# Kernel tuning notes

Measured on AMD Instinct MI355X. Metric: run time of the kernel, lower is better.

The kernel has to match this reference:

```python
import jax, jax.numpy as jnp
import numpy as np

NUM_HEADS = 8
H_DIM = 24
COORDS_DIM = 3
NUM_W_PER_DIST = 8
BLOCK_SIZE = 128
N_HASHES = 3
N = 32768
HASH_DIM = H_DIM + (COORDS_DIM - 1) + 2  # q/k augmented with RPE coordinate terms


def layernorm(x, g, b, eps=1e-5):
    mu = x.mean(-1, keepdims=True)
    var = ((x - mu) ** 2).mean(-1, keepdims=True)
    return (x - mu) * jax.lax.rsqrt(var + eps) * g + b


def setup_inputs() -> dict:
    key = jax.random.key(0)
    ks = jax.random.split(key, 16)
    d, H = H_DIM, NUM_HEADS
    s = lambda i, shape, scale: jax.random.normal(ks[i], shape, jnp.float32) * scale
    return {
        "x": s(0, (N, d), 1.0),
        "coords": jax.random.uniform(ks[1], (N, COORDS_DIM), jnp.float32),
        "norm1_g": jnp.ones((d,), jnp.float32),
        "norm1_b": jnp.zeros((d,), jnp.float32),
        "Wq": s(2, (d, H * d), d ** -0.5),
        "Wk": s(3, (d, H * d), d ** -0.5),
        "Wv": s(4, (d, H * d), d ** -0.5),
        "w_rpe_W": s(5, (H * d, (COORDS_DIM - 1) * NUM_W_PER_DIST), 0.3),
        "Wo": s(6, (H * d, d), (H * d) ** -0.5),
        "bo": jnp.zeros((d,), jnp.float32),
        "norm2_g": jnp.ones((d,), jnp.float32),
        "norm2_b": jnp.zeros((d,), jnp.float32),
        "ff_W1": s(7, (d, d), d ** -0.5),
        "ff_b1": jnp.zeros((d,), jnp.float32),
        "ff_W2": s(8, (d, d), d ** -0.5),
        "ff_b2": jnp.zeros((d,), jnp.float32),
        "alphas": s(9, (N_HASHES, H, HASH_DIM), 1.0),  # E2LSH projection vectors
    }


def hept_attention(q, k, v, coords, w_rpe_W, alphas):
    # q,k,v: [n, H*d]. HEPT: fold RPE exp(-w*||dp||^2) into augmented q/k, then
    # n_hashes rounds of LSH sort + block-local attention, combined by softmax
    # over each round's log-normalizer (Reformer-style).
    n = q.shape[0]
    H, d, B = NUM_HEADS, H_DIM, BLOCK_SIZE
    nb = n // B
    q = q.reshape(n, H, d).transpose(1, 0, 2) * (d ** -0.5)  # [H,n,d]
    k = k.reshape(n, H, d).transpose(1, 0, 2)
    v = v.reshape(n, H, d).transpose(1, 0, 2)
    # per-head non-negative distance weights from w_rpe (mixture collapsed)
    Wm = w_rpe_W.reshape(H, d, COORDS_DIM - 1, NUM_W_PER_DIST)
    w = jnp.mean(Wm, axis=(1, 3)) ** 2                        # [H, c-1]
    p = coords[:, 1:]                                          # [n, c-1]
    sqn = jnp.einsum("hc,nc,nc->hn", w, p, p)                # w*||p||^2
    qp = jnp.sqrt(2.0) * jnp.sqrt(w)[:, None, :] * p[None]     # [H,n,c-1]
    ones = jnp.ones((H, n, 1), q.dtype)
    # q_hat.k_hat = q.k + 2*w*p_i.p_j - w|p_i|^2 - w|p_j|^2 = q.k - w*||p_i-p_j||^2
    q_hat = jnp.concatenate([q, qp, -sqn[..., None], ones], -1)  # [H,n,HASH_DIM]
    k_hat = jnp.concatenate([k, qp, ones, -sqn[..., None]], -1)
    outs, zs = [], []
    for r in range(N_HASHES):
        a = alphas[r]                                          # [H, HASH_DIM]
        iq = jnp.argsort(jnp.einsum("hne,he->hn", q_hat, a), -1)
        ik = jnp.argsort(jnp.einsum("hne,he->hn", k_hat, a), -1)
        qs = jnp.take_along_axis(q_hat, iq[..., None], 1).reshape(H, nb, B, -1)
        ks = jnp.take_along_axis(k_hat, ik[..., None], 1).reshape(H, nb, B, -1)
        vs = jnp.take_along_axis(v, ik[..., None], 1).reshape(H, nb, B, d)
        logits = jnp.einsum("hbqe,hbke->hbqk", qs, ks)         # [H,nb,B,B]
        z = jax.nn.logsumexp(logits, -1).reshape(H, n)
        o = jnp.einsum("hbqk,hbkd->hbqd", jax.nn.softmax(logits, -1), vs).reshape(H, n, d)
        inv = jnp.argsort(iq, -1)                              # unsort to input order
        outs.append(jnp.take_along_axis(o, inv[..., None], 1))
        zs.append(jnp.take_along_axis(z, inv, 1))
    wts = jax.nn.softmax(jnp.stack(zs), axis=0)[..., None]     # [R,H,n,1]
    out = (jnp.stack(outs) * wts).sum(0)                       # [H,n,d]
    return out.transpose(1, 0, 2).reshape(n, H * d)


def reference(x, coords, norm1_g, norm1_b, Wq, Wk, Wv, w_rpe_W, Wo, bo,
              norm2_g, norm2_b, ff_W1, ff_b1, ff_W2, ff_b2, alphas):
    xn = layernorm(x, norm1_g, norm1_b)
    q, k, v = xn @ Wq, xn @ Wk, xn @ Wv
    aggr = hept_attention(q, k, v, coords, w_rpe_W, alphas) @ Wo + bo
    x = x + aggr  # dropout is identity in eval mode
    h = layernorm(x, norm2_g, norm2_b)
    ff = jax.nn.relu(h @ ff_W1 + ff_b1) @ ff_W2 + ff_b2
    return x + ff
```

## Files before the change

kernel.cpp:

```cpp
#include <hip/hip_runtime.h>
#include <math.h>

#define NPT 32768
#define NH 8
#define HD 24
#define EDIM 28
#define NHASH 3
#define NSEG 48
#define NRH 24

typedef unsigned long long u64;
typedef unsigned short ushort;
typedef __attribute__((__vector_size__(8 * sizeof(short)))) short bf16x8;
typedef __attribute__((__vector_size__(4 * sizeof(float)))) float floatx4;

__device__ __forceinline__ ushort f2bf(float f) {
    unsigned u = __float_as_uint(f);
    unsigned r = u + 0x7FFF + ((u >> 16) & 1);
    return (ushort)(r >> 16);
}
__device__ __forceinline__ float us2f(ushort u) {
    return __uint_as_float(((unsigned)u) << 16);
}

__global__ __launch_bounds__(256) void k0b(
    const float* __restrict__ wrpe, const float* __restrict__ Wq,
    const float* __restrict__ Wk, const float* __restrict__ alphas,
    double* __restrict__ w64, double* __restrict__ cqp64,
    double* __restrict__ Aq, double* __restrict__ Ak, double* __restrict__ ct) {
    __shared__ double sw[16], sc[16];
    int t = threadIdx.x;
    if (t < 16) {
        int h = t >> 1, c = t & 1;
        double s = 0.0;
        for (int i = 0; i < 24; i++)
            for (int j = 0; j < 8; j++)
                s += (double)wrpe[(h * 24 + i) * 16 + c * 8 + j];
        double m = s / 192.0;
        sw[t] = m * m;
        sc[t] = sqrt(2.0) * fabs(m);
        w64[t] = sw[t];
        cqp64[t] = sc[t];
    }
    __syncthreads();
    const double QSCALE = 1.0 / sqrt(24.0);
    for (int idx = t; idx < 24 * NRH; idx += 256) {
        int i = idx / NRH, rh = idx % NRH;
        int h = rh & 7;
        double aq = 0.0, ak = 0.0;
        for (int e = 0; e < 24; e++) {
            double al = (double)alphas[rh * 28 + e];
            aq += (double)Wq[i * 192 + h * 24 + e] * al;
            ak += (double)Wk[i * 192 + h * 24 + e] * al;
        }
        Aq[idx] = aq * QSCALE;
        Ak[idx] = ak;
    }
    if (t < NRH) {
        int h = t & 7;
        ct[t * 4 + 0] = (double)alphas[t * 28 + 24] * sc[h * 2 + 0];
        ct[t * 4 + 1] = (double)alphas[t * 28 + 25] * sc[h * 2 + 1];
        ct[t * 4 + 2] = (double)alphas[t * 28 + 26];
        ct[t * 4 + 3] = (double)alphas[t * 28 + 27];
    }
}

__global__ __launch_bounds__(256) void k1b(
    const float* __restrict__ x, const float* __restrict__ g,
    const float* __restrict__ b, float* __restrict__ xnf) {
    __shared__ float sGB[48];
    int t = threadIdx.x;
    if (t < 24) { sGB[t] = g[t]; sGB[24 + t] = b[t]; }
    __syncthreads();
    int wv = t >> 6, l = t & 63;
    int half = l >> 5, e = l & 31;
    for (int it = 0; it < 8; it++) {
        int n = blockIdx.x * 64 + it * 8 + wv * 2 + half;
        float xv = (e < 24) ? x[(u64)n * 24 + e] : 0.f;
        float s = xv;
        s += __shfl_xor(s, 1); s += __shfl_xor(s, 2); s += __shfl_xor(s, 4);
        s += __shfl_xor(s, 8); s += __shfl_xor(s, 16);
        float mu = s * (1.0f / 24.0f);
        float d = (e < 24) ? (xv - mu) : 0.f;
        float v = d * d;
        v += __shfl_xor(v, 1); v += __shfl_xor(v, 2); v += __shfl_xor(v, 4);
        v += __shfl_xor(v, 8); v += __shfl_xor(v, 16);
        float rstd = 1.0f / sqrtf(v * (1.0f / 24.0f) + 1e-5f);
        if (e < 24) xnf[(u64)n * 24 + e] = d * rstd * sGB[e] + sGB[24 + e];
    }
}

__global__ __launch_bounds__(512) void k2s(
    const float* __restrict__ x, const float* __restrict__ n1g,
    const float* __restrict__ n1b, const float* __restrict__ coords,
    const double* __restrict__ Aq, const double* __restrict__ Ak,
    const double* __restrict__ ct, const double* __restrict__ w64,
    u64* __restrict__ keys) {
    __shared__ double sA[2][24][NRH];
    __shared__ double sCt[NRH][4];
    __shared__ double sW64[16];
    __shared__ double sGB[48];
    __shared__ double sXn[8][24];
    int t = threadIdx.x;
    for (int i = t; i < 24 * NRH; i += 512) sA[0][i / NRH][i % NRH] = Aq[i];
    for (int i = t; i < 24 * NRH; i += 512) sA[1][i / NRH][i % NRH] = Ak[i];
    for (int i = t; i < NRH * 4; i += 512) sCt[i / 4][i % 4] = ct[i];
    if (t < 16) sW64[t] = w64[t];
    if (t < 24) { sGB[t] = (double)n1g[t]; sGB[24 + t] = (double)n1b[t]; }
    __syncthreads();
    int wv = t >> 6, l = t & 63;
    for (int g = 0; g < 8; g++) {
        int n = blockIdx.x * 64 + g * 8 + wv;
        double xv = (l < 24) ? (double)x[(u64)n * 24 + l] : 0.0;
        double s = xv;
        s += __shfl_xor(s, 1); s += __shfl_xor(s, 2); s += __shfl_xor(s, 4);
        s += __shfl_xor(s, 8); s += __shfl_xor(s, 16);
        double mu = s / 24.0;
        double d = (l < 24) ? (xv - mu) : 0.0;
        double v2 = d * d;
        v2 += __shfl_xor(v2, 1); v2 += __shfl_xor(v2, 2); v2 += __shfl_xor(v2, 4);
        v2 += __shfl_xor(v2, 8); v2 += __shfl_xor(v2, 16);
        double rstd = 1.0 / sqrt(v2 / 24.0 + 1e-5);
        if (l < 24) sXn[wv][l] = d * rstd * sGB[l] + sGB[24 + l];
        double p0 = (double)coords[(u64)n * 3 + 1];
        double p1 = (double)coords[(u64)n * 3 + 2];
        if (l < 2 * NRH) {
            int qk = l / NRH, rh = l % NRH;
            int h = rh & 7;
            double sqn = sW64[2 * h] * p0 * p0 + sW64[2 * h + 1] * p1 * p1;
            double acc = sCt[rh][0] * p0 + sCt[rh][1] * p1;
            acc += qk ? (sCt[rh][2] - sqn * sCt[rh][3]) : (sCt[rh][3] - sqn * sCt[rh][2]);
            for (int i = 0; i < 24; i++) acc += sXn[wv][i] * sA[qk][i][rh];
            u64 u = (u64)__double_as_longlong(acc);
            if (u >> 63) u = ~u; else u |= 0x8000000000000000ULL;
            u64 key = (u & ~(u64)32767) | (u64)n;
            keys[(u64)l * NPT + n] = key;
        }
    }
}

#define K2P_PTS 64
__global__ __launch_bounds__(640) void k2p(
    const float* __restrict__ xnf,
    const float* __restrict__ Wq, const float* __restrict__ Wk,
    const float* __restrict__ Wv, const float* __restrict__ coords,
    const double* __restrict__ w64, const double* __restrict__ cqp64,
    ushort* __restrict__ qhatB, ushort* __restrict__ khatB, ushort* __restrict__ varrB) {
    int t = threadIdx.x;
    int n0 = blockIdx.x * K2P_PTS;
    if (t < 576) {
        int m = t / 192, jj = t % 192;
        const float* W = (m == 0) ? Wq : ((m == 1) ? Wk : Wv);
        float wc[24];
#pragma unroll
        for (int i = 0; i < 24; i++) wc[i] = W[i * 192 + jj];
        const float scale = (m == 0) ? (float)(1.0 / sqrt(24.0)) : 1.0f;
        int h = jj / 24, e = jj % 24;
        ushort* outp = (m == 0) ? qhatB : ((m == 1) ? khatB : varrB);
        ushort* obase = outp + (u64)h * NPT * 32 + e;
        for (int p = 0; p < K2P_PTS; p++) {
            int n = n0 + p;
            const float* xr = xnf + (u64)n * 24;
            float acc = 0.f;
#pragma unroll
            for (int i = 0; i < 24; i++) acc += xr[i] * wc[i];
            obase[(u64)n * 32] = f2bf(acc * scale);
        }
    } else {
        int l = t - 576;
        int h2 = l >> 3, e2 = 24 + (l & 7);
        double c0 = cqp64[h2 * 2], c1 = cqp64[h2 * 2 + 1];
        double wa = w64[h2 * 2], wb = w64[h2 * 2 + 1];
        ushort* qb = qhatB + (u64)h2 * NPT * 32 + e2;
        ushort* kb = khatB + (u64)h2 * NPT * 32 + e2;
        for (int p = 0; p < K2P_PTS; p++) {
            int n = n0 + p;
            double p0 = (double)coords[(u64)n * 3 + 1];
            double p1 = (double)coords[(u64)n * 3 + 2];
            float qv, kv;
            if (e2 < 26) {
                int c = e2 - 24;
                float qp = (float)((c ? c1 : c0) * (c ? p1 : p0));
                qv = qp; kv = qp;
            } else if (e2 < 28) {
                double sqn = wa * p0 * p0 + wb * p1 * p1;
                if (e2 == 26) { qv = (float)(-sqn); kv = 1.0f; }
                else          { qv = 1.0f; kv = (float)(-sqn); }
            } else {
                qv = 0.0f; kv = 0.0f;
            }
            qb[(u64)n * 32] = f2bf(qv);
            kb[(u64)n * 32] = f2bf(kv);
        }
    }
}

__device__ __forceinline__ u64 shflx64(u64 v, int d) {
    int lo = __shfl_xor((int)(unsigned)v, d);
    int hi = __shfl_xor((int)(unsigned)(v >> 32), d);
    return ((u64)(unsigned)hi << 32) | (unsigned)lo;
}
__device__ __forceinline__ void cswap(u64& a, u64& b, bool up) {
    if ((a > b) == up) { u64 tmp = a; a = b; b = tmp; }
}
__device__ __forceinline__ u64* sslot(u64* s, int i) {
    int a = i << 3;
    a ^= ((a >> 9) & 7) << 4;
    return (u64*)((char*)s + a);
}
__device__ __forceinline__ void reg_passes(u64 e[8], int ib, int K, int jmax) {
    for (int j = jmax; j >= 1; j >>= 1) {
#pragma unroll
        for (int k = 0; k < 8; k++)
            if ((k & j) == 0) cswap(e[k], e[k | j], ((ib + k) & K) == 0);
    }
}
__device__ __forceinline__ void shfl_passes(u64 e[8], int t, int segoff, int K, int jhi, int jlo) {
    for (int j = jhi; j >= jlo; j >>= 1) {
        int d = j >> 3;
        bool lower = (t & d) == 0;
        bool up = ((segoff + ((t & ~d) << 3)) & K) == 0;
        bool keepmin = (lower == up);
#pragma unroll
        for (int k = 0; k < 8; k++) {
            u64 o = shflx64(e[k], d);
            bool ownsm = e[k] < o;
            e[k] = (ownsm == keepmin) ? e[k] : o;
        }
    }
}

__global__ __launch_bounds__(1024) void sort_local_full(u64* keys) {
    __shared__ u64 s[8192];
    int t = threadIdx.x;
    u64 gbase = (u64)blockIdx.x * 8192;
    int segoff = (int)(gbase & 32767);
    int ib = segoff + t * 8;
    u64 e[8];
#pragma unroll
    for (int k = 0; k < 8; k++) e[k] = keys[gbase + t * 8 + k];
    reg_passes(e, ib, 2, 1);
    reg_passes(e, ib, 4, 2);
    reg_passes(e, ib, 8, 4);
    for (int K = 16; K <= 512; K <<= 1) {
        shfl_passes(e, t, segoff, K, K >> 1, 8);
        reg_passes(e, ib, K, 4);
    }
#pragma unroll
    for (int k = 0; k < 8; k++) *sslot(s, t * 8 + k) = e[k];
    __syncthreads();
    for (int K = 1024; K <= 8192; K <<= 1) {
        for (int j = K >> 1; j >= 512; j >>= 1) {
            for (int p = t; p < 4096; p += 1024) {
                int i = ((p & ~(j - 1)) << 1) | (p & (j - 1));
                int i2 = i | j;
                bool up = (((segoff + i) & K) == 0);
                u64 a = *sslot(s, i), b = *sslot(s, i2);
                if ((a > b) == up) { *sslot(s, i) = b; *sslot(s, i2) = a; }
            }
            __syncthreads();
        }
#pragma unroll
        for (int k = 0; k < 8; k++) e[k] = *sslot(s, t * 8 + k);
        shfl_passes(e, t, segoff, K, 256, 8);
        reg_passes(e, ib, K, 4);
        if (K < 8192) {
#pragma unroll
            for (int k = 0; k < 8; k++) *sslot(s, t * 8 + k) = e[k];
            __syncthreads();
        } else {
#pragma unroll
            for (int k = 0; k < 8; k++) keys[gbase + t * 8 + k] = e[k];
        }
    }
}

__global__ __launch_bounds__(1024) void sort_local_tail(u64* keys, int K, int minj) {
    __shared__ u64 s[8192];
    int t = threadIdx.x;
    u64 gbase = (u64)blockIdx.x * 8192;
    int segoff = (int)(gbase & 32767);
    int ib = segoff + t * 8;
    for (int i = t; i < 8192; i += 1024) *sslot(s, i) = keys[gbase + i];
    __syncthreads();
    for (int j = 4096; j >= 512; j >>= 1) {
        for (int p = t; p < 4096; p += 1024) {
            int i = ((p & ~(j - 1)) << 1) | (p & (j - 1));
            int i2 = i | j;
            bool up = (((segoff + i) & K) == 0);
            u64 a = *sslot(s, i), b = *sslot(s, i2);
            if ((a > b) == up) { *sslot(s, i) = b; *sslot(s, i2) = a; }
        }
        __syncthreads();
    }
    u64 e[8];
#pragma unroll
    for (int k = 0; k < 8; k++) e[k] = *sslot(s, t * 8 + k);
    shfl_passes(e, t, segoff, K, 256, minj >= 8 ? minj : 8);
    if (minj < 8) reg_passes(e, ib, K, 4);
#pragma unroll
    for (int k = 0; k < 8; k++) keys[gbase + t * 8 + k] = e[k];
}

__global__ void sort_global_pass(u64* keys, int k, int j) {
    int p = blockIdx.x * blockDim.x + threadIdx.x;
    if (p >= NSEG * NPT / 2) return;
    int i = ((p & ~(j - 1)) << 1) | (p & (j - 1));
    int l2 = i | j;
    bool up = (((i & 32767) & k) == 0);
    u64 a = keys[i], b = keys[l2];
    if ((a > b) == up) { keys[i] = b; keys[l2] = a; }
}

__global__ void sort_global2(u64* keys) {
    int p = blockIdx.x * blockDim.x + threadIdx.x;
    if (p >= NSEG * 8192) return;
    int seg = p >> 13, c = p & 8191;
    u64 base = (u64)seg * 32768 + c;
    u64 e0 = keys[base];
    u64 e1 = keys[base + 8192];
    u64 e2 = keys[base + 16384];
    u64 e3 = keys[base + 24576];
    u64 tmp;
    if (e0 > e2) { tmp = e0; e0 = e2; e2 = tmp; }
    if (e1 > e3) { tmp = e1; e1 = e3; e3 = tmp; }
    if (e0 > e1) { tmp = e0; e0 = e1; e1 = tmp; }
    if (e2 > e3) { tmp = e2; e2 = e3; e3 = tmp; }
    keys[base] = e0;
    keys[base + 8192] = e1;
    keys[base + 16384] = e2;
    keys[base + 24576] = e3;
}

#define VT_STRIDE 136
#define P_STRIDE 72
__global__ __launch_bounds__(256, 4) void k3_attn(
    const u64* __restrict__ keys, const ushort* __restrict__ qhatB,
    const ushort* __restrict__ khatB, const ushort* __restrict__ varrB,
    ushort* __restrict__ ozB) {
    int rh3 = blockIdx.x % 24;
    int b = blockIdx.x / 24;
    int h = rh3 & 7, r = rh3 >> 3;
    __shared__ __align__(16) char smem[6528 + 18432 + 1024];
    short* sVt = (short*)smem;
    short* sP  = (short*)(smem + 6528);
    int* qidx  = (int*)(smem + 6528 + 18432);
    int* kidx  = qidx + 128;
    int t = threadIdx.x;
    int segQ = r * 8 + h, segK = 24 + r * 8 + h;
    if (t < 128) {
        qidx[t] = (int)(keys[(u64)segQ * NPT + b * 128 + t] & 32767ULL);
    } else {
        int i = t - 128;
        kidx[i] = (int)(keys[(u64)segK * NPT + b * 128 + i] & 32767ULL);
    }
    __syncthreads();

    int wave = t >> 6, L = t & 63;
    int quad = L >> 4, n16 = L & 15;

    const bf16x8* Qg = (const bf16x8*)(qhatB + (u64)h * NPT * 32);
    const bf16x8* Kg = (const bf16x8*)(khatB + (u64)h * NPT * 32);
    bf16x8 afr[2];
#pragma unroll
    for (int rtg = 0; rtg < 2; rtg++) {
        int qi = qidx[wave * 32 + rtg * 16 + n16];
        afr[rtg] = Qg[(u64)qi * 4 + quad];
    }
    bf16x8 bfr[8];
#pragma unroll
    for (int ct = 0; ct < 8; ct++) {
        int ki = kidx[ct * 16 + n16];
        bfr[ct] = Kg[(u64)ki * 4 + quad];
    }
    if (t < 128) {
        int ki = kidx[t];
        const bf16x8* vr = (const bf16x8*)(varrB + ((u64)h * NPT + ki) * 32);
        bf16x8 v0 = vr[0], v1 = vr[1], v2 = vr[2];
#pragma unroll
        for (int e = 0; e < 8; e++) {
            sVt[e * VT_STRIDE + t]        = v0[e];
            sVt[(8 + e) * VT_STRIDE + t]  = v1[e];
            sVt[(16 + e) * VT_STRIDE + t] = v2[e];
        }
    }
    __syncthreads();

    floatx4 acc[2][8];
#pragma unroll
    for (int rtg = 0; rtg < 2; rtg++)
#pragma unroll
        for (int ct = 0; ct < 8; ct++)
            acc[rtg][ct] = (floatx4){0.f, 0.f, 0.f, 0.f};
#pragma unroll
    for (int ct = 0; ct < 8; ct++) {
#pragma unroll
        for (int rtg = 0; rtg < 2; rtg++)
            acc[rtg][ct] = __builtin_amdgcn_mfma_f32_16x16x32_bf16(afr[rtg], bfr[ct], acc[rtg][ct], 0, 0, 0);
    }

    float mrow[2][4], srow[2][4];
#pragma unroll
    for (int rtg = 0; rtg < 2; rtg++) {
#pragma unroll
        for (int rg = 0; rg < 4; rg++) {
            float m = -1e30f;
#pragma unroll
            for (int ct = 0; ct < 8; ct++) m = fmaxf(m, acc[rtg][ct][rg]);
            m = fmaxf(m, __shfl_xor(m, 1));
            m = fmaxf(m, __shfl_xor(m, 2));
            m = fmaxf(m, __shfl_xor(m, 4));
            m = fmaxf(m, __shfl_xor(m, 8));
            mrow[rtg][rg] = m;
            float s = 0.0f;
            int row = wave * 32 + rtg * 16 + quad * 4 + rg;
#pragma unroll
            for (int ct = 0; ct < 8; ct++) {
                float p = __expf(acc[rtg][ct][rg] - m);
                s += p;
                if (ct < 4) sP[row * P_STRIDE + ct * 16 + n16] = (short)f2bf(p);
            }
            s += __shfl_xor(s, 1);
            s += __shfl_xor(s, 2);
            s += __shfl_xor(s, 4);
            s += __shfl_xor(s, 8);
            srow[rtg][rg] = s;
        }
    }

    floatx4 occ[2][2];
#pragma unroll
    for (int rtg = 0; rtg < 2; rtg++)
#pragma unroll
        for (int ct2 = 0; ct2 < 2; ct2++)
            occ[rtg][ct2] = (floatx4){0.f, 0.f, 0.f, 0.f};
#pragma unroll
    for (int ks = 0; ks < 2; ks++) {
        bf16x8 bv[2], av[2];
#pragma unroll
        for (int ct2 = 0; ct2 < 2; ct2++)
            bv[ct2] = *(const bf16x8*)(sVt + (ct2 * 16 + n16) * VT_STRIDE + ks * 32 + quad * 8);
#pragma unroll
        for (int rtg = 0; rtg < 2; rtg++)
            av[rtg] = *(const bf16x8*)(sP + (wave * 32 + rtg * 16 + n16) * P_STRIDE + ks * 32 + quad * 8);
#pragma unroll
        for (int rtg = 0; rtg < 2; rtg++)
#pragma unroll
            for (int ct2 = 0; ct2 < 2; ct2++)
                occ[rtg][ct2] = __builtin_amdgcn_mfma_f32_16x16x32_bf16(av[rtg], bv[ct2], occ[rtg][ct2], 0, 0, 0);
    }
#pragma unroll
    for (int rtg = 0; rtg < 2; rtg++) {
#pragma unroll
        for (int rg = 0; rg < 4; rg++) {
            int row = wave * 32 + rtg * 16 + quad * 4 + rg;
#pragma unroll
            for (int ct = 4; ct < 8; ct++) {
                float p = __expf(acc[rtg][ct][rg] - mrow[rtg][rg]);
                sP[row * P_STRIDE + (ct - 4) * 16 + n16] = (short)f2bf(p);
            }
        }
    }
#pragma unroll
    for (int ks = 2; ks < 4; ks++) {
        bf16x8 bv[2], av[2];
#pragma unroll
        for (int ct2 = 0; ct2 < 2; ct2++)
            bv[ct2] = *(const bf16x8*)(sVt + (ct2 * 16 + n16) * VT_STRIDE + ks * 32 + quad * 8);
#pragma unroll
        for (int rtg = 0; rtg < 2; rtg++)
            av[rtg] = *(const bf16x8*)(sP + (wave * 32 + rtg * 16 + n16) * P_STRIDE + (ks - 2) * 32 + quad * 8);
#pragma unroll
        for (int rtg = 0; rtg < 2; rtg++)
#pragma unroll
            for (int ct2 = 0; ct2 < 2; ct2++)
                occ[rtg][ct2] = __builtin_amdgcn_mfma_f32_16x16x32_bf16(av[rtg], bv[ct2], occ[rtg][ct2], 0, 0, 0);
    }

#pragma unroll
    for (int rtg = 0; rtg < 2; rtg++) {
#pragma unroll
        for (int rg = 0; rg < 4; rg++) {
            int row = wave * 32 + rtg * 16 + quad * 4 + rg;
            int oi = qidx[row];
            float inv = 1.0f / srow[rtg][rg];
            ushort* orow = ozB + ((u64)segQ * NPT + oi) * 32;
#pragma unroll
            for (int ct2 = 0; ct2 < 2; ct2++) {
                int col = ct2 * 16 + n16;
                if (col < 24) orow[col] = f2bf(occ[rtg][ct2][rg] * inv);
            }
            if (n16 == 0)
                *(float*)(orow + 24) = mrow[rtg][rg] + __logf(srow[rtg][rg]);
        }
    }
}

#define K4PTS 32
#define AT_STR 196
__global__ __launch_bounds__(256) void k4_final(
    const ushort* __restrict__ ozB,
    const float* __restrict__ x,
    const float* __restrict__ Wo, const float* __restrict__ bo,
    const float* __restrict__ g2, const float* __restrict__ b2,
    const float* __restrict__ W1, const float* __restrict__ b1f,
    const float* __restrict__ W2, const float* __restrict__ b2f,
    float* __restrict__ out) {
    __shared__ __align__(16) float sWoT[24][AT_STR];
    __shared__ float sW1[24 * 24], sW2[24 * 24];
    __shared__ float sB[5 * 24];
    __shared__ __align__(16) float attn[K4PTS][AT_STR];
    __shared__ float xrow[K4PTS][25];
    __shared__ float h2row[K4PTS][25];
    __shared__ float ffrow[K4PTS][25];
    int t = threadIdx.x;
    int base = blockIdx.x * K4PTS;
    for (int i = t; i < 4608; i += 256) sWoT[i % 24][i / 24] = Wo[i];
    for (int i = t; i < 576; i += 256) { sW1[i] = W1[i]; sW2[i] = W2[i]; }
    if (t < 24) {
        sB[t] = bo[t]; sB[24 + t] = g2[t]; sB[48 + t] = b2[t];
        sB[72 + t] = b1f[t]; sB[96 + t] = b2f[t];
    }
    {
        int p = t >> 3, h = t & 7;
        int n = base + p;
        const ushort* r0 = ozB + ((u64)(0 * 8 + h) * NPT + n) * 32;
        const ushort* r1 = ozB + ((u64)(1 * 8 + h) * NPT + n) * 32;
        const ushort* r2 = ozB + ((u64)(2 * 8 + h) * NPT + n) * 32;
        float z0 = *(const float*)(r0 + 24);
        float z1 = *(const float*)(r1 + 24);
        float z2 = *(const float*)(r2 + 24);
        float zm = fmaxf(z0, fmaxf(z1, z2));
        float e0 = __expf(z0 - zm), e1 = __expf(z1 - zm), e2 = __expf(z2 - zm);
        float inv = 1.0f / (e0 + e1 + e2);
        float w0 = e0 * inv, w1 = e1 * inv, w2 = e2 * inv;
#pragma unroll
        for (int e = 0; e < 24; e++)
            attn[p][h * 24 + e] = w0 * us2f(r0[e]) + w1 * us2f(r1[e]) + w2 * us2f(r2[e]);
    }
    __syncthreads();
    int p = t >> 3, oe = t & 7;
    int n = base + p;
    {
        const floatx4* ap = (const floatx4*)&attn[p][0];
        const floatx4* w0p = (const floatx4*)&sWoT[oe][0];
        const floatx4* w1p = (const floatx4*)&sWoT[oe + 8][0];
        const floatx4* w2p = (const floatx4*)&sWoT[oe + 16][0];
        floatx4 A0 = {0.f, 0.f, 0.f, 0.f}, A1 = A0, A2 = A0;
        for (int ii = 0; ii < 48; ii++) {
            floatx4 av = ap[ii];
            A0 += av * w0p[ii];
            A1 += av * w1p[ii];
            A2 += av * w2p[ii];
        }
        float a0 = A0[0] + A0[1] + A0[2] + A0[3];
        float a1 = A1[0] + A1[1] + A1[2] + A1[3];
        float a2 = A2[0] + A2[1] + A2[2] + A2[3];
        xrow[p][oe]      = x[n * 24 + oe]      + a0 + sB[oe];
        xrow[p][oe + 8]  = x[n * 24 + oe + 8]  + a1 + sB[oe + 8];
        xrow[p][oe + 16] = x[n * 24 + oe + 16] + a2 + sB[oe + 16];
    }
    float mu, rstd;
    {
        float s = xrow[p][oe] + xrow[p][oe + 8] + xrow[p][oe + 16];
        s += __shfl_xor(s, 1); s += __shfl_xor(s, 2); s += __shfl_xor(s, 4);
        mu = s / 24.0f;
        float v0 = xrow[p][oe] - mu, v1 = xrow[p][oe + 8] - mu, v2 = xrow[p][oe + 16] - mu;
        float v = v0 * v0 + v1 * v1 + v2 * v2;
        v += __shfl_xor(v, 1); v += __shfl_xor(v, 2); v += __shfl_xor(v, 4);
        rstd = 1.0f / sqrtf(v / 24.0f + 1e-5f);
    }
    h2row[p][oe]      = (xrow[p][oe] - mu)      * rstd * sB[24 + oe]      + sB[48 + oe];
    h2row[p][oe + 8]  = (xrow[p][oe + 8] - mu)  * rstd * sB[24 + oe + 8]  + sB[48 + oe + 8];
    h2row[p][oe + 16] = (xrow[p][oe + 16] - mu) * rstd * sB[24 + oe + 16] + sB[48 + oe + 16];
    {
        float a0 = sB[72 + oe], a1 = sB[72 + oe + 8], a2 = sB[72 + oe + 16];
        for (int i = 0; i < 24; i++) {
            float hi = h2row[p][i];
            a0 += hi * sW1[i * 24 + oe];
            a1 += hi * sW1[i * 24 + oe + 8];
            a2 += hi * sW1[i * 24 + oe + 16];
        }
        ffrow[p][oe]      = fmaxf(a0, 0.f);
        ffrow[p][oe + 8]  = fmaxf(a1, 0.f);
        ffrow[p][oe + 16] = fmaxf(a2, 0.f);
    }
    {
        float a0 = sB[96 + oe], a1 = sB[96 + oe + 8], a2 = sB[96 + oe + 16];
        for (int i = 0; i < 24; i++) {
            float fi = ffrow[p][i];
            a0 += fi * sW2[i * 24 + oe];
            a1 += fi * sW2[i * 24 + oe + 8];
            a2 += fi * sW2[i * 24 + oe + 16];
        }
        out[n * 24 + oe]      = xrow[p][oe]      + a0;
        out[n * 24 + oe + 8]  = xrow[p][oe + 8]  + a1;
        out[n * 24 + oe + 16] = xrow[p][oe + 16] + a2;
    }
}

extern "C" void kernel_launch(void* const* d_in, const int* in_sizes, int n_in,
                              void* d_out, int out_size, void* d_ws, size_t ws_size,
                              hipStream_t stream) {
    const float* x      = (const float*)d_in[0];
    const float* coords = (const float*)d_in[1];
    const float* n1g    = (const float*)d_in[2];
    const float* n1b    = (const float*)d_in[3];
    const float* Wq     = (const float*)d_in[4];
    const float* Wk     = (const float*)d_in[5];
    const float* Wv     = (const float*)d_in[6];
    const float* wrpe   = (const float*)d_in[7];
    const float* Wo     = (const float*)d_in[8];
    const float* bo     = (const float*)d_in[9];
    const float* n2g    = (const float*)d_in[10];
    const float* n2b    = (const float*)d_in[11];
    const float* W1     = (const float*)d_in[12];
    const float* b1     = (const float*)d_in[13];
    const float* W2     = (const float*)d_in[14];
    const float* b2     = (const float*)d_in[15];
    const float* alphas = (const float*)d_in[16];

    char* ws = (char*)d_ws;
    size_t off = 0;
    auto alloc = [&](size_t bytes) -> void* {
        void* p = ws + off;
        off = (off + bytes + 255) & ~(size_t)255;
        return p;
    };
    double* w64   = (double*)alloc(256);
    double* cqp   = (double*)alloc(256);
    double* Aq    = (double*)alloc(24 * NRH * 8);
    double* Ak    = (double*)alloc(24 * NRH * 8);
    double* ct    = (double*)alloc(NRH * 4 * 8);
    float*  xnf   = (float*)alloc((size_t)NPT * 24 * 4);
    ushort* qhatB = (ushort*)alloc((size_t)NH * NPT * 32 * 2);
    ushort* khatB = (ushort*)alloc((size_t)NH * NPT * 32 * 2);
    ushort* varrB = (ushort*)alloc((size_t)NH * NPT * 32 * 2);
    u64*    keys  = (u64*)alloc((size_t)NSEG * NPT * 8);
    ushort* ozB   = (ushort*)alloc((size_t)NHASH * NH * NPT * 32 * 2);
    if (off > ws_size) return;

    k0b<<<1, 256, 0, stream>>>(wrpe, Wq, Wk, alphas, w64, cqp, Aq, Ak, ct);
    k1b<<<NPT / 64, 256, 0, stream>>>(x, n1g, n1b, xnf);
    k2s<<<NPT / 64, 512, 0, stream>>>(x, n1g, n1b, coords, Aq, Ak, ct, w64, keys);
    k2p<<<NPT / K2P_PTS, 640, 0, stream>>>(xnf, Wq, Wk, Wv, coords, w64, cqp,
                                           qhatB, khatB, varrB);
    sort_local_full<<<192, 1024, 0, stream>>>(keys);
    sort_global_pass<<<3072, 256, 0, stream>>>(keys, 16384, 8192);
    sort_local_tail<<<192, 1024, 0, stream>>>(keys, 16384, 1);
    sort_global2<<<NSEG * 8192 / 256, 256, 0, stream>>>(keys);
    sort_local_tail<<<192, 1024, 0, stream>>>(keys, 32768, 128);
    k3_attn<<<256 * 8 * 3, 256, 0, stream>>>(keys, qhatB, khatB, varrB, ozB);
    k4_final<<<NPT / K4PTS, 256, 0, stream>>>(ozB, x, Wo, bo, n2g, n2b,
                                              W1, b1, W2, b2, (float*)d_out);
}
```

Measured before the change: 321.1 us.

## Fuse layernorm into key kernel, fold global sort pass into local tail, vectorize FFN

Removes the separate layernorm kernel k1b by having k2s also write the float normalized activations. The bitonic global compare-exchange pass with j=8192 is folded into the following local tail kernel: each block loads its own chunk and the partner chunk and keeps the min or max. The FFN matmuls in k4_final use transposed, padded weight tiles and floatx4 dot products. The result is two fewer launches and less global traffic, at the cost of redundant partner reads in the fused sort and a different float summation order in the FFN.

```diff
diff --git a/kernel.cpp b/kernel.cpp
--- a/kernel.cpp
+++ b/kernel.cpp
@@ -65,37 +65,12 @@
     }
 }
 
-__global__ __launch_bounds__(256) void k1b(
-    const float* __restrict__ x, const float* __restrict__ g,
-    const float* __restrict__ b, float* __restrict__ xnf) {
-    __shared__ float sGB[48];
-    int t = threadIdx.x;
-    if (t < 24) { sGB[t] = g[t]; sGB[24 + t] = b[t]; }
-    __syncthreads();
-    int wv = t >> 6, l = t & 63;
-    int half = l >> 5, e = l & 31;
-    for (int it = 0; it < 8; it++) {
-        int n = blockIdx.x * 64 + it * 8 + wv * 2 + half;
-        float xv = (e < 24) ? x[(u64)n * 24 + e] : 0.f;
-        float s = xv;
-        s += __shfl_xor(s, 1); s += __shfl_xor(s, 2); s += __shfl_xor(s, 4);
-        s += __shfl_xor(s, 8); s += __shfl_xor(s, 16);
-        float mu = s * (1.0f / 24.0f);
-        float d = (e < 24) ? (xv - mu) : 0.f;
-        float v = d * d;
-        v += __shfl_xor(v, 1); v += __shfl_xor(v, 2); v += __shfl_xor(v, 4);
-        v += __shfl_xor(v, 8); v += __shfl_xor(v, 16);
-        float rstd = 1.0f / sqrtf(v * (1.0f / 24.0f) + 1e-5f);
-        if (e < 24) xnf[(u64)n * 24 + e] = d * rstd * sGB[e] + sGB[24 + e];
-    }
-}
-
 __global__ __launch_bounds__(512) void k2s(
     const float* __restrict__ x, const float* __restrict__ n1g,
     const float* __restrict__ n1b, const float* __restrict__ coords,
     const double* __restrict__ Aq, const double* __restrict__ Ak,
     const double* __restrict__ ct, const double* __restrict__ w64,
-    u64* __restrict__ keys) {
+    u64* __restrict__ keys, float* __restrict__ xnf) {
     __shared__ double sA[2][24][NRH];
     __shared__ double sCt[NRH][4];
     __shared__ double sW64[16];
@@ -121,7 +96,11 @@
         v2 += __shfl_xor(v2, 1); v2 += __shfl_xor(v2, 2); v2 += __shfl_xor(v2, 4);
         v2 += __shfl_xor(v2, 8); v2 += __shfl_xor(v2, 16);
         double rstd = 1.0 / sqrt(v2 / 24.0 + 1e-5);
-        if (l < 24) sXn[wv][l] = d * rstd * sGB[l] + sGB[24 + l];
+        if (l < 24) {
+            double xn = d * rstd * sGB[l] + sGB[24 + l];
+            sXn[wv][l] = xn;
+            xnf[(u64)n * 24 + l] = (float)xn;
+        }
         double p0 = (double)coords[(u64)n * 3 + 1];
         double p1 = (double)coords[(u64)n * 3 + 2];
         if (l < 2 * NRH) {
@@ -275,14 +254,24 @@
     }
 }
 
-__global__ __launch_bounds__(1024) void sort_local_tail(u64* keys, int K, int minj) {
+__global__ __launch_bounds__(1024) void sort_tail1_fused(u64* keys) {
     __shared__ u64 s[8192];
     int t = threadIdx.x;
     u64 gbase = (u64)blockIdx.x * 8192;
+    u64 pbase = gbase ^ 8192ULL;
+    int ci = (int)((gbase >> 13) & 3);
+    bool keepmin = (ci == 0) || (ci == 3);
     int segoff = (int)(gbase & 32767);
     int ib = segoff + t * 8;
-    for (int i = t; i < 8192; i += 1024) *sslot(s, i) = keys[gbase + i];
-    __syncthreads();
+    for (int i = t; i < 8192; i += 1024) {
+        u64 a = keys[gbase + i];
+        u64 b = keys[pbase + i];
+        u64 mn = a < b ? a : b;
+        u64 mx = a < b ? b : a;
+        *sslot(s, i) = keepmin ? mn : mx;
+    }
+    __syncthreads();
+    const int K = 16384;
     for (int j = 4096; j >= 512; j >>= 1) {
         for (int p = t; p < 4096; p += 1024) {
             int i = ((p & ~(j - 1)) << 1) | (p & (j - 1));
@@ -296,20 +285,37 @@
     u64 e[8];
 #pragma unroll
     for (int k = 0; k < 8; k++) e[k] = *sslot(s, t * 8 + k);
+    shfl_passes(e, t, segoff, K, 256, 8);
+    reg_passes(e, ib, K, 4);
+#pragma unroll
+    for (int k = 0; k < 8; k++) keys[gbase + t * 8 + k] = e[k];
+}
+
+__global__ __launch_bounds__(1024) void sort_local_tail(u64* keys, int K, int minj) {
+    __shared__ u64 s[8192];
+    int t = threadIdx.x;
+    u64 gbase = (u64)blockIdx.x * 8192;
+    int segoff = (int)(gbase & 32767);
+    int ib = segoff + t * 8;
+    for (int i = t; i < 8192; i += 1024) *sslot(s, i) = keys[gbase + i];
+    __syncthreads();
+    for (int j = 4096; j >= 512; j >>= 1) {
+        for (int p = t; p < 4096; p += 1024) {
+            int i = ((p & ~(j - 1)) << 1) | (p & (j - 1));
+            int i2 = i | j;
+            bool up = (((segoff + i) & K) == 0);
+            u64 a = *sslot(s, i), b = *sslot(s, i2);
+            if ((a > b) == up) { *sslot(s, i) = b; *sslot(s, i2) = a; }
+        }
+        __syncthreads();
+    }
+    u64 e[8];
+#pragma unroll
+    for (int k = 0; k < 8; k++) e[k] = *sslot(s, t * 8 + k);
     shfl_passes(e, t, segoff, K, 256, minj >= 8 ? minj : 8);
     if (minj < 8) reg_passes(e, ib, K, 4);
 #pragma unroll
     for (int k = 0; k < 8; k++) keys[gbase + t * 8 + k] = e[k];
-}
-
-__global__ void sort_global_pass(u64* keys, int k, int j) {
-    int p = blockIdx.x * blockDim.x + threadIdx.x;
-    if (p >= NSEG * NPT / 2) return;
-    int i = ((p & ~(j - 1)) << 1) | (p & (j - 1));
-    int l2 = i | j;
-    bool up = (((i & 32767) & k) == 0);
-    u64 a = keys[i], b = keys[l2];
-    if ((a > b) == up) { keys[i] = b; keys[l2] = a; }
 }
 
 __global__ void sort_global2(u64* keys) {
@@ -498,6 +504,7 @@
 
 #define K4PTS 32
 #define AT_STR 196
+#define W_STR 28
 __global__ __launch_bounds__(256) void k4_final(
     const ushort* __restrict__ ozB,
     const float* __restrict__ x,
@@ -507,19 +514,30 @@
     const float* __restrict__ W2, const float* __restrict__ b2f,
     float* __restrict__ out) {
     __shared__ __align__(16) float sWoT[24][AT_STR];
-    __shared__ float sW1[24 * 24], sW2[24 * 24];
+    __shared__ __align__(16) float sW1T[24][W_STR], sW2T[24][W_STR];
     __shared__ float sB[5 * 24];
     __shared__ __align__(16) float attn[K4PTS][AT_STR];
     __shared__ float xrow[K4PTS][25];
-    __shared__ float h2row[K4PTS][25];
-    __shared__ float ffrow[K4PTS][25];
+    __shared__ __align__(16) float h2row[K4PTS][W_STR];
+    __shared__ __align__(16) float ffrow[K4PTS][W_STR];
     int t = threadIdx.x;
     int base = blockIdx.x * K4PTS;
     for (int i = t; i < 4608; i += 256) sWoT[i % 24][i / 24] = Wo[i];
-    for (int i = t; i < 576; i += 256) { sW1[i] = W1[i]; sW2[i] = W2[i]; }
+    for (int i = t; i < 576; i += 256) {
+        sW1T[i % 24][i / 24] = W1[i];
+        sW2T[i % 24][i / 24] = W2[i];
+    }
     if (t < 24) {
         sB[t] = bo[t]; sB[24 + t] = g2[t]; sB[48 + t] = b2[t];
         sB[72 + t] = b1f[t]; sB[96 + t] = b2f[t];
+    }
+    if (t < K4PTS * 4) {
+        int p = t >> 2, c = 24 + (t & 3);
+        h2row[p][c] = 0.f; ffrow[p][c] = 0.f;
+    }
+    if (t < 24 * 4) {
+        int rr = t >> 2, c = 24 + (t & 3);
+        sW1T[rr][c] = 0.f; sW2T[rr][c] = 0.f;
     }
     {
         int p = t >> 3, h = t & 7;
@@ -574,28 +592,38 @@
     h2row[p][oe + 8]  = (xrow[p][oe + 8] - mu)  * rstd * sB[24 + oe + 8]  + sB[48 + oe + 8];
     h2row[p][oe + 16] = (xrow[p][oe + 16] - mu) * rstd * sB[24 + oe + 16] + sB[48 + oe + 16];
     {
-        float a0 = sB[72 + oe], a1 = sB[72 + oe + 8], a2 = sB[72 + oe + 16];
-        for (int i = 0; i < 24; i++) {
-            float hi = h2row[p][i];
-            a0 += hi * sW1[i * 24 + oe];
-            a1 += hi * sW1[i * 24 + oe + 8];
-            a2 += hi * sW1[i * 24 + oe + 16];
-        }
-        ffrow[p][oe]      = fmaxf(a0, 0.f);
-        ffrow[p][oe + 8]  = fmaxf(a1, 0.f);
-        ffrow[p][oe + 16] = fmaxf(a2, 0.f);
+        const floatx4* hp = (const floatx4*)&h2row[p][0];
+        const floatx4* w0p = (const floatx4*)&sW1T[oe][0];
+        const floatx4* w1p = (const floatx4*)&sW1T[oe + 8][0];
+        const floatx4* w2p = (const floatx4*)&sW1T[oe + 16][0];
+        floatx4 A0 = {0.f, 0.f, 0.f, 0.f}, A1 = A0, A2 = A0;
+#pragma unroll
+        for (int ii = 0; ii < 6; ii++) {
+            floatx4 hv = hp[ii];
+            A0 += hv * w0p[ii];
+            A1 += hv * w1p[ii];
+            A2 += hv * w2p[ii];
+        }
+        ffrow[p][oe]      = fmaxf(A0[0]+A0[1]+A0[2]+A0[3] + sB[72 + oe], 0.f);
+        ffrow[p][oe + 8]  = fmaxf(A1[0]+A1[1]+A1[2]+A1[3] + sB[72 + oe + 8], 0.f);
+        ffrow[p][oe + 16] = fmaxf(A2[0]+A2[1]+A2[2]+A2[3] + sB[72 + oe + 16], 0.f);
     }
     {
-        float a0 = sB[96 + oe], a1 = sB[96 + oe + 8], a2 = sB[96 + oe + 16];
-        for (int i = 0; i < 24; i++) {
-            float fi = ffrow[p][i];
-            a0 += fi * sW2[i * 24 + oe];
-            a1 += fi * sW2[i * 24 + oe + 8];
-            a2 += fi * sW2[i * 24 + oe + 16];
-        }
-        out[n * 24 + oe]      = xrow[p][oe]      + a0;
-        out[n * 24 + oe + 8]  = xrow[p][oe + 8]  + a1;
-        out[n * 24 + oe + 16] = xrow[p][oe + 16] + a2;
+        const floatx4* fp = (const floatx4*)&ffrow[p][0];
+        const floatx4* w0p = (const floatx4*)&sW2T[oe][0];
+        const floatx4* w1p = (const floatx4*)&sW2T[oe + 8][0];
+        const floatx4* w2p = (const floatx4*)&sW2T[oe + 16][0];
+        floatx4 A0 = {0.f, 0.f, 0.f, 0.f}, A1 = A0, A2 = A0;
+#pragma unroll
+        for (int ii = 0; ii < 6; ii++) {
+            floatx4 fv = fp[ii];
+            A0 += fv * w0p[ii];
+            A1 += fv * w1p[ii];
+            A2 += fv * w2p[ii];
+        }
+        out[n * 24 + oe]      = xrow[p][oe]      + A0[0]+A0[1]+A0[2]+A0[3] + sB[96 + oe];
+        out[n * 24 + oe + 8]  = xrow[p][oe + 8]  + A1[0]+A1[1]+A1[2]+A1[3] + sB[96 + oe + 8];
+        out[n * 24 + oe + 16] = xrow[p][oe + 16] + A2[0]+A2[1]+A2[2]+A2[3] + sB[96 + oe + 16];
     }
 }
 
@@ -641,13 +669,11 @@
     if (off > ws_size) return;
 
     k0b<<<1, 256, 0, stream>>>(wrpe, Wq, Wk, alphas, w64, cqp, Aq, Ak, ct);
-    k1b<<<NPT / 64, 256, 0, stream>>>(x, n1g, n1b, xnf);
-    k2s<<<NPT / 64, 512, 0, stream>>>(x, n1g, n1b, coords, Aq, Ak, ct, w64, keys);
+    k2s<<<NPT / 64, 512, 0, stream>>>(x, n1g, n1b, coords, Aq, Ak, ct, w64, keys, xnf);
     k2p<<<NPT / K2P_PTS, 640, 0, stream>>>(xnf, Wq, Wk, Wv, coords, w64, cqp,
                                            qhatB, khatB, varrB);
     sort_local_full<<<192, 1024, 0, stream>>>(keys);
-    sort_global_pass<<<3072, 256, 0, stream>>>(keys, 16384, 8192);
-    sort_local_tail<<<192, 1024, 0, stream>>>(keys, 16384, 1);
+    sort_tail1_fused<<<192, 1024, 0, stream>>>(keys);
     sort_global2<<<NSEG * 8192 / 256, 256, 0, stream>>>(keys);
     sort_local_tail<<<192, 1024, 0, stream>>>(keys, 32768, 128);
     k3_attn<<<256 * 8 * 3, 256, 0, stream>>>(keys, qhatB, khatB, varrB, ozB);
```

After: 307.6 us. 1.04x faster.
